# Optimization experiments

Hardware: AMD Instinct MI355X
Metric: run time of the kernel (lower is better)

Reference implementation:

```python
import jax, jax.numpy as jnp
import numpy as np

B, N, D, H = 4, 1024, 1024, 16
DH = D // H
SCALE = jnp.sqrt(jnp.float32(DH))


def setup_inputs() -> dict:
    key = jax.random.key(0)
    ks = jax.random.split(key, 12)
    Q = jax.random.normal(ks[0], (B, N, D), dtype=jnp.float32)
    K = jax.random.normal(ks[1], (B, N, D), dtype=jnp.float32)
    V = jax.random.normal(ks[2], (B, N, D), dtype=jnp.float32)
    mask = jax.random.bernoulli(ks[3], 0.1, (B, H, N, N))
    w_scale = 0.02
    Wq = jax.random.normal(ks[4], (D, D), dtype=jnp.float32) * w_scale
    Wk = jax.random.normal(ks[5], (D, D), dtype=jnp.float32) * w_scale
    Wv = jax.random.normal(ks[6], (D, D), dtype=jnp.float32) * w_scale
    Wo = jax.random.normal(ks[7], (D, D), dtype=jnp.float32) * w_scale
    bq = jax.random.normal(ks[8], (D,), dtype=jnp.float32) * w_scale
    bk = jax.random.normal(ks[9], (D,), dtype=jnp.float32) * w_scale
    bv = jax.random.normal(ks[10], (D,), dtype=jnp.float32) * w_scale
    bo = jax.random.normal(ks[11], (D,), dtype=jnp.float32) * w_scale
    return {"Q": Q, "K": K, "V": V, "mask": mask,
            "Wq": Wq, "bq": bq, "Wk": Wk, "bk": bk,
            "Wv": Wv, "bv": bv, "Wo": Wo, "bo": bo}


def _split_heads(x):
    # [b, n, (h d)] -> [b, h, n, d]
    b, n, _ = x.shape
    return x.reshape(b, n, H, DH).transpose(0, 2, 1, 3)


def reference(Q, K, V, mask, Wq, bq, Wk, bk, Wv, bv, Wo, bo):
    # torch nn.Linear: y = x @ W.T + b
    q = _split_heads(Q @ Wq.T + bq)
    k = _split_heads(K @ Wk.T + bk)
    v = _split_heads(V @ Wv.T + bv)
    # scores: [b, h, n, n]
    scores = jnp.einsum('bhnd,bhmd->bhnm', q, k) / SCALE
    scores = jnp.where(mask, jnp.float32(-1e10), scores)
    weights = jax.nn.softmax(scores, axis=-1)
    attn = jnp.einsum('bhnm,bhmd->bhnd', weights, v)
    x = attn.transpose(0, 2, 1, 3).reshape(Q.shape[0], Q.shape[1], D)
    x = x @ Wo.T + bo
    return (x, weights)
```

## Files before the change

### kernel.cpp

```cpp
#include <hip/hip_runtime.h>


#define SEQ   1024
#define D_DIM 1024
#define HEADS 16
#define DHEAD 64
#define BATCH 4

typedef __attribute__((ext_vector_type(8))) short bhalf8;
typedef __attribute__((ext_vector_type(4))) float floatx4;

static __device__ __forceinline__ unsigned short f2b(float f) {
    unsigned int u = __float_as_uint(f);
    u += 0x7FFFu + ((u >> 16) & 1u);
    return (unsigned short)(u >> 16);
}

__global__ __launch_bounds__(256) void detect_mask_kernel(const uint4* __restrict__ m,
                                                          int* __restrict__ flag) {
    __shared__ int found;
    if (threadIdx.x == 0) found = 0;
    __syncthreads();
    unsigned int bad = 0;
#pragma unroll
    for (int i = 0; i < 16; ++i) {
        uint4 w = m[threadIdx.x + i * 256];
        unsigned int a = w.x, b = w.y, c = w.z, d = w.w;
        bad |= (a != 0u && a != 1u && a != 0x3F800000u);
        bad |= (b != 0u && b != 1u && b != 0x3F800000u);
        bad |= (c != 0u && c != 1u && c != 0x3F800000u);
        bad |= (d != 0u && d != 1u && d != 0x3F800000u);
    }
    if (bad) atomicOr(&found, 1);
    __syncthreads();
    if (threadIdx.x == 0) *flag = found;
}

__global__ __launch_bounds__(256) void mask_pack(const void* __restrict__ mask,
                                                 const int* __restrict__ mflagp,
                                                 unsigned int* __restrict__ bits) {
    const size_t idx = (size_t)blockIdx.x * 256 + threadIdx.x;
    unsigned int w = 0;
    if (*mflagp) {
        const uint4* p = (const uint4*)mask + idx * 2;
        uint4 a = p[0], b = p[1];
        unsigned int d[8] = {a.x, a.y, a.z, a.w, b.x, b.y, b.z, b.w};
#pragma unroll
        for (int i = 0; i < 8; ++i) {
            unsigned int x = d[i];
            w |= (((x & 0x000000FFu) != 0u) ? 1u : 0u) << (i * 4 + 0);
            w |= (((x & 0x0000FF00u) != 0u) ? 1u : 0u) << (i * 4 + 1);
            w |= (((x & 0x00FF0000u) != 0u) ? 1u : 0u) << (i * 4 + 2);
            w |= (((x & 0xFF000000u) != 0u) ? 1u : 0u) << (i * 4 + 3);
        }
    } else {
        const uint4* p = (const uint4*)mask + idx * 8;
#pragma unroll
        for (int i = 0; i < 8; ++i) {
            uint4 a = p[i];
            w |= (a.x ? 1u : 0u) << (i * 4 + 0);
            w |= (a.y ? 1u : 0u) << (i * 4 + 1);
            w |= (a.z ? 1u : 0u) << (i * 4 + 2);
            w |= (a.w ? 1u : 0u) << (i * 4 + 3);
        }
    }
    bits[idx] = w;
}

template <int AMODE, int OMODE>
__global__ __launch_bounds__(256) void gemm_bt(const void* __restrict__ Aptr,
                                               const float* __restrict__ W,
                                               const float* __restrict__ bias,
                                               void* __restrict__ Out) {
    __shared__ unsigned short Al[128 * 72];
    __shared__ unsigned short Bl[128 * 72];

    const int tid = threadIdx.x;
    const int lane = tid & 63, wid = tid >> 6;
    const int lr = lane & 15, lq = lane >> 4;
    const int wm = (wid & 1) * 64, wn = (wid >> 1) * 64;
    const int rowBase = blockIdx.y * 128;
    const int colBase = blockIdx.x * 128;

    floatx4 acc[4][4];
    for (int mi = 0; mi < 4; ++mi)
        for (int ni = 0; ni < 4; ++ni)
            for (int r = 0; r < 4; ++r) acc[mi][ni][r] = 0.f;

    for (int k0 = 0; k0 < D_DIM; k0 += 64) {
        if (AMODE == 0) {
            const float* A = (const float*)Aptr;
            for (int i = 0; i < 8; ++i) {
                int id = tid + i * 256;
                int r = id >> 4, c4 = id & 15;
                float4 f = *(const float4*)&A[(size_t)(rowBase + r) * D_DIM + k0 + c4 * 4];
                ushort4 h;
                h.x = f2b(f.x); h.y = f2b(f.y); h.z = f2b(f.z); h.w = f2b(f.w);
                *(ushort4*)&Al[r * 72 + c4 * 4] = h;
            }
        } else {
            const unsigned short* A = (const unsigned short*)Aptr;
            for (int i = 0; i < 4; ++i) {
                int id = tid + i * 256;
                int r = id >> 3, c8 = id & 7;
                *(uint4*)&Al[r * 72 + c8 * 8] =
                    *(const uint4*)&A[(size_t)(rowBase + r) * D_DIM + k0 + c8 * 8];
            }
        }
        for (int i = 0; i < 8; ++i) {
            int id = tid + i * 256;
            int r = id >> 4, c4 = id & 15;
            float4 f = *(const float4*)&W[(size_t)(colBase + r) * D_DIM + k0 + c4 * 4];
            ushort4 h;
            h.x = f2b(f.x); h.y = f2b(f.y); h.z = f2b(f.z); h.w = f2b(f.w);
            *(ushort4*)&Bl[r * 72 + c4 * 4] = h;
        }
        __syncthreads();
        for (int ks = 0; ks < 2; ++ks) {
            bhalf8 af[4], bfr[4];
            for (int mi = 0; mi < 4; ++mi)
                af[mi] = *(const bhalf8*)&Al[(wm + mi * 16 + lr) * 72 + ks * 32 + lq * 8];
            for (int ni = 0; ni < 4; ++ni)
                bfr[ni] = *(const bhalf8*)&Bl[(wn + ni * 16 + lr) * 72 + ks * 32 + lq * 8];
            for (int mi = 0; mi < 4; ++mi)
                for (int ni = 0; ni < 4; ++ni)
                    acc[mi][ni] = __builtin_amdgcn_mfma_f32_16x16x32_bf16(af[mi], bfr[ni],
                                                                          acc[mi][ni], 0, 0, 0);
        }
        __syncthreads();
    }

    for (int mi = 0; mi < 4; ++mi) {
        for (int ni = 0; ni < 4; ++ni) {
            int col = colBase + wn + ni * 16 + lr;
            float bv = bias[col];
            for (int r = 0; r < 4; ++r) {
                int m = rowBase + wm + mi * 16 + lq * 4 + r;
                float v = acc[mi][ni][r] + bv;
                if (OMODE == 0) {
                    unsigned short* o = (unsigned short*)Out;
                    int b = m >> 10, n = m & 1023, h = col >> 6, dh = col & 63;
                    o[(((size_t)(b * HEADS + h)) << 16) + (n << 6) + dh] = f2b(v);
                } else {
                    float* o = (float*)Out;
                    o[(size_t)m * D_DIM + col] = v;
                }
            }
        }
    }
}

__global__ __launch_bounds__(256, 4) void attn_kernel(const unsigned short* __restrict__ qh,
                                                      const unsigned short* __restrict__ kh,
                                                      const unsigned short* __restrict__ vh,
                                                      const unsigned int* __restrict__ bits,
                                                      float* __restrict__ wout,
                                                      unsigned short* __restrict__ attnb) {
    __shared__ unsigned short ql[64 * 64];
    __shared__ unsigned short kl[64 * 64];
    __shared__ unsigned short vtl[64 * 64];
    __shared__ unsigned short pl[64 * 64];
    __shared__ unsigned int maskw[64 * 32];

    const int tid = threadIdx.x;
    const int lane = tid & 63, wid = tid >> 6;
    const int lr = lane & 15, lq = lane >> 4;

    const int wg = blockIdx.x;
    const int xcd = wg & 7, tt = wg >> 3;
    const int bh = ((tt >> 4) << 3) | xcd;
    const int row0 = (tt & 15) << 6;

    const size_t hoff = (size_t)bh << 16;
    const unsigned short* qp = qh + hoff;
    const unsigned short* kp = kh + hoff;
    const unsigned short* vp = vh + hoff;

#pragma unroll
    for (int i = 0; i < 2; ++i) {
        int id = tid + i * 256;
        int r = id >> 3, c8 = id & 7;
        *(uint4*)&ql[r * 64 + ((c8 ^ (r & 7)) << 3)] =
            *(const uint4*)&qp[((size_t)(row0 + r) << 6) + c8 * 8];
    }
    {
        const unsigned int* src = bits + ((size_t)bh * SEQ + row0) * 32;
#pragma unroll
        for (int i = 0; i < 2; ++i) {
            int id = tid + i * 256;
            *(uint4*)&maskw[id * 4] = *(const uint4*)&src[id * 4];
        }
    }

    uint4 kreg0, kreg1, vreg0, vreg1;
#define LOADK(j)                                                                          \
    {                                                                                     \
        kreg0 = *(const uint4*)&kp[((size_t)(((j) << 6) + (tid >> 3)) << 6) + (tid & 7) * 8];        \
        kreg1 = *(const uint4*)&kp[((size_t)(((j) << 6) + ((tid + 256) >> 3)) << 6) + (tid & 7) * 8]; \
    }
#define STOREK                                                                  \
    {                                                                           \
        int r0 = tid >> 3, c0 = tid & 7, r1 = (tid + 256) >> 3;                 \
        *(uint4*)&kl[r0 * 64 + ((c0 ^ (r0 & 7)) << 3)] = kreg0;                 \
        *(uint4*)&kl[r1 * 64 + ((c0 ^ (r1 & 7)) << 3)] = kreg1;                 \
    }
#define LOADV(j)                                                                          \
    {                                                                                     \
        vreg0 = *(const uint4*)&vp[((size_t)(((j) << 6) + (tid & 63)) << 6) + ((tid >> 6) * 8)];      \
        vreg1 = *(const uint4*)&vp[((size_t)(((j) << 6) + (tid & 63)) << 6) + ((tid >> 6) * 8 + 32)]; \
    }
#define STOREV                                                                  \
    {                                                                           \
        int n0 = tid & 63, d0 = (tid >> 6) * 8, d1 = d0 + 32;                   \
        const unsigned short* e0 = (const unsigned short*)&vreg0;               \
        const unsigned short* e1 = (const unsigned short*)&vreg1;               \
        _Pragma("unroll") for (int t = 0; t < 8; ++t) {                         \
            vtl[(d0 + t) * 64 + (n0 ^ (t << 3))] = e0[t];                       \
            vtl[(d1 + t) * 64 + (n0 ^ (t << 3))] = e1[t];                       \
        }                                                                       \
    }

    float m_l[4], l_l[4];
#pragma unroll
    for (int r = 0; r < 4; ++r) { m_l[r] = -3e38f; l_l[r] = 0.f; }

    LOADK(0);
    for (int j = 0; j < 16; ++j) {
        __syncthreads();
        STOREK;
        if (j < 15) LOADK(j + 1);
        __syncthreads();

        floatx4 sacc[4];
#pragma unroll
        for (int c = 0; c < 4; ++c)
#pragma unroll
            for (int r = 0; r < 4; ++r) sacc[c][r] = 0.f;
#pragma unroll
        for (int ks = 0; ks < 2; ++ks) {
            int arow = wid * 16 + lr;
            bhalf8 a = *(const bhalf8*)&ql[arow * 64 + (((ks * 4 + lq) ^ (lr & 7)) << 3)];
#pragma unroll
            for (int c = 0; c < 4; ++c) {
                int brow = c * 16 + lr;
                bhalf8 bb = *(const bhalf8*)&kl[brow * 64 + (((ks * 4 + lq) ^ (lr & 7)) << 3)];
                sacc[c] = __builtin_amdgcn_mfma_f32_16x16x32_bf16(a, bb, sacc[c], 0, 0, 0);
            }
        }
        unsigned int w0[4], w1[4];
#pragma unroll
        for (int r = 0; r < 4; ++r) {
            int row = wid * 16 + lq * 4 + r;
            w0[r] = maskw[row * 32 + j * 2];
            w1[r] = maskw[row * 32 + j * 2 + 1];
        }
#pragma unroll
        for (int c = 0; c < 4; ++c) {
            int sh = lr + ((c & 1) << 4);
#pragma unroll
            for (int r = 0; r < 4; ++r) {
                unsigned int w = (c >> 1) ? w1[r] : w0[r];
                float s = sacc[c][r] * 0.125f;
                sacc[c][r] = ((w >> sh) & 1u) ? -1e10f : s;
            }
        }
#pragma unroll
        for (int r = 0; r < 4; ++r) {
            float mx = fmaxf(fmaxf(sacc[0][r], sacc[1][r]), fmaxf(sacc[2][r], sacc[3][r]));
            float mn = fmaxf(m_l[r], mx);
            float sv = __expf(sacc[0][r] - mn) + __expf(sacc[1][r] - mn) +
                       __expf(sacc[2][r] - mn) + __expf(sacc[3][r] - mn);
            l_l[r] = l_l[r] * __expf(m_l[r] - mn) + sv;
            m_l[r] = mn;
        }
    }
#pragma unroll
    for (int o = 1; o < 16; o <<= 1) {
#pragma unroll
        for (int r = 0; r < 4; ++r) {
            float mo = __shfl_xor(m_l[r], o);
            float lo = __shfl_xor(l_l[r], o);
            float mn = fmaxf(m_l[r], mo);
            l_l[r] = l_l[r] * __expf(m_l[r] - mn) + lo * __expf(mo - mn);
            m_l[r] = mn;
        }
    }
    float invl[4];
#pragma unroll
    for (int r = 0; r < 4; ++r) invl[r] = 1.f / l_l[r];

    floatx4 oacc[4];
#pragma unroll
    for (int c = 0; c < 4; ++c)
#pragma unroll
        for (int r = 0; r < 4; ++r) oacc[c][r] = 0.f;
    const size_t wrowbase = ((size_t)bh * SEQ + row0) * SEQ;

    LOADK(0);
    LOADV(0);
    for (int j = 0; j < 16; ++j) {
        __syncthreads();
        STOREK;
        STOREV;
        if (j < 15) { LOADK(j + 1); LOADV(j + 1); }
        __syncthreads();

        floatx4 sacc[4];
#pragma unroll
        for (int c = 0; c < 4; ++c)
#pragma unroll
            for (int r = 0; r < 4; ++r) sacc[c][r] = 0.f;
#pragma unroll
        for (int ks = 0; ks < 2; ++ks) {
            int arow = wid * 16 + lr;
            bhalf8 a = *(const bhalf8*)&ql[arow * 64 + (((ks * 4 + lq) ^ (lr & 7)) << 3)];
#pragma unroll
            for (int c = 0; c < 4; ++c) {
                int brow = c * 16 + lr;
                bhalf8 bb = *(const bhalf8*)&kl[brow * 64 + (((ks * 4 + lq) ^ (lr & 7)) << 3)];
                sacc[c] = __builtin_amdgcn_mfma_f32_16x16x32_bf16(a, bb, sacc[c], 0, 0, 0);
            }
        }
        unsigned int w0[4], w1[4];
#pragma unroll
        for (int r = 0; r < 4; ++r) {
            int row = wid * 16 + lq * 4 + r;
            w0[r] = maskw[row * 32 + j * 2];
            w1[r] = maskw[row * 32 + j * 2 + 1];
        }
#pragma unroll
        for (int c = 0; c < 4; ++c) {
            int sh = lr + ((c & 1) << 4);
            int col = (j << 6) + c * 16 + lr;
#pragma unroll
            for (int r = 0; r < 4; ++r) {
                unsigned int w = (c >> 1) ? w1[r] : w0[r];
                int row = wid * 16 + lq * 4 + r;
                float s = sacc[c][r] * 0.125f;
                if ((w >> sh) & 1u) s = -1e10f;
                float p = __expf(s - m_l[r]) * invl[r];
                wout[wrowbase + (size_t)row * SEQ + col] = p;
                pl[row * 64 + ((c * 16 + lr) ^ ((row & 7) << 3))] = f2b(p);
            }
        }
#pragma unroll
        for (int ks = 0; ks < 2; ++ks) {
            int arow = wid * 16 + lr;
            bhalf8 a = *(const bhalf8*)&pl[arow * 64 + (((ks * 4 + lq) ^ (lr & 7)) << 3)];
#pragma unroll
            for (int c = 0; c < 4; ++c) {
                int brow = c * 16 + lr;
                bhalf8 bb = *(const bhalf8*)&vtl[brow * 64 + (((ks * 4 + lq) ^ (lr & 7)) << 3)];
                oacc[c] = __builtin_amdgcn_mfma_f32_16x16x32_bf16(a, bb, oacc[c], 0, 0, 0);
            }
        }
    }

    const int b = bh >> 4, h = bh & 15;
#pragma unroll
    for (int c = 0; c < 4; ++c) {
        int colg = h * 64 + c * 16 + lr;
#pragma unroll
        for (int r = 0; r < 4; ++r) {
            int n = row0 + wid * 16 + lq * 4 + r;
            attnb[(size_t)(b * SEQ + n) * D_DIM + colg] = f2b(oacc[c][r]);
        }
    }
#undef LOADK
#undef STOREK
#undef LOADV
#undef STOREV
}

extern "C" void kernel_launch(void* const* d_in, const int* in_sizes, int n_in,
                              void* d_out, int out_size, void* d_ws, size_t ws_size,
                              hipStream_t stream) {
    const float* Q = (const float*)d_in[0];
    const float* K = (const float*)d_in[1];
    const float* V = (const float*)d_in[2];
    const void* mask = d_in[3];
    const float* Wq = (const float*)d_in[4];
    const float* bq = (const float*)d_in[5];
    const float* Wk = (const float*)d_in[6];
    const float* bk = (const float*)d_in[7];
    const float* Wv = (const float*)d_in[8];
    const float* bv = (const float*)d_in[9];
    const float* Wo = (const float*)d_in[10];
    const float* bo = (const float*)d_in[11];

    char* ws = (char*)d_ws;
    int* mflag = (int*)ws;
    unsigned short* qhb = (unsigned short*)(ws + 256);
    unsigned short* khb = qhb + 4194304;
    unsigned short* vhb = khb + 4194304;
    unsigned short* attnb = vhb + 4194304;
    unsigned int* bitsbuf = (unsigned int*)(attnb + 4194304);

    float* xout = (float*)d_out;
    float* wout = xout + (size_t)BATCH * SEQ * D_DIM;

    dim3 blk(256);
    detect_mask_kernel<<<1, blk, 0, stream>>>((const uint4*)mask, mflag);
    mask_pack<<<dim3(8192), blk, 0, stream>>>(mask, mflag, bitsbuf);

    dim3 g(8, 32);
    gemm_bt<0, 0><<<g, blk, 0, stream>>>(Q, Wq, bq, qhb);
    gemm_bt<0, 0><<<g, blk, 0, stream>>>(K, Wk, bk, khb);
    gemm_bt<0, 0><<<g, blk, 0, stream>>>(V, Wv, bv, vhb);

    attn_kernel<<<dim3(1024), blk, 0, stream>>>(qhb, khb, vhb, bitsbuf, wout, attnb);

    gemm_bt<1, 1><<<g, blk, 0, stream>>>(attnb, Wo, bo, xout);
}
```

Measured before the change: 714.2 us.

## Pre-cast GEMM operands to bf16 and stream tiles with direct global-to-LDS loads

New measurement: 645.8 us. 9.6% less time.

```diff
diff --git a/kernel.cpp b/kernel.cpp
--- a/kernel.cpp
+++ b/kernel.cpp
@@ -10,10 +10,17 @@
 typedef __attribute__((ext_vector_type(8))) short bhalf8;
 typedef __attribute__((ext_vector_type(4))) float floatx4;
 
+typedef __attribute__((address_space(1))) const void GlobCV;
+typedef __attribute__((address_space(3))) void LdsV;
+
 static __device__ __forceinline__ unsigned short f2b(float f) {
     unsigned int u = __float_as_uint(f);
     u += 0x7FFFu + ((u >> 16) & 1u);
     return (unsigned short)(u >> 16);
+}
+
+static __device__ __forceinline__ void gload16(const void* g, void* l) {
+    __builtin_amdgcn_global_load_lds((GlobCV*)g, (LdsV*)l, 16, 0, 0);
 }
 
 __global__ __launch_bounds__(256) void detect_mask_kernel(const uint4* __restrict__ m,
@@ -67,13 +74,48 @@
     bits[idx] = w;
 }
 
-template <int AMODE, int OMODE>
-__global__ __launch_bounds__(256) void gemm_bt(const void* __restrict__ Aptr,
-                                               const float* __restrict__ W,
-                                               const float* __restrict__ bias,
-                                               void* __restrict__ Out) {
-    __shared__ unsigned short Al[128 * 72];
-    __shared__ unsigned short Bl[128 * 72];
+__global__ __launch_bounds__(256) void cast_f2b_all(const float* __restrict__ Q,
+                                                    const float* __restrict__ K,
+                                                    const float* __restrict__ V,
+                                                    const float* __restrict__ Wq,
+                                                    const float* __restrict__ Wk,
+                                                    const float* __restrict__ Wv,
+                                                    const float* __restrict__ Wo,
+                                                    unsigned short* __restrict__ Ab,
+                                                    unsigned short* __restrict__ Wb) {
+    const int y = blockIdx.y;
+    const float* src;
+    unsigned short* dst;
+    int nblocks;
+    if (y < 3) {
+        src = (y == 0) ? Q : (y == 1) ? K : V;
+        dst = Ab + ((size_t)y << 22);
+        nblocks = 2048;
+    } else {
+        src = (y == 3) ? Wq : (y == 4) ? Wk : (y == 5) ? Wv : Wo;
+        dst = Wb + ((size_t)(y - 3) << 20);
+        nblocks = 512;
+    }
+    if (blockIdx.x >= (unsigned)nblocks) return;
+    const size_t i = ((size_t)blockIdx.x * 256 + threadIdx.x) * 8;
+    float4 f0 = *(const float4*)&src[i];
+    float4 f1 = *(const float4*)&src[i + 4];
+    ushort4 h0, h1;
+    h0.x = f2b(f0.x); h0.y = f2b(f0.y); h0.z = f2b(f0.z); h0.w = f2b(f0.w);
+    h1.x = f2b(f1.x); h1.y = f2b(f1.y); h1.z = f2b(f1.z); h1.w = f2b(f1.w);
+    *(ushort4*)&dst[i] = h0;
+    *(ushort4*)&dst[i + 4] = h1;
+}
+
+template <int OMODE>
+__global__ __launch_bounds__(256) void gemm_lds(const unsigned short* __restrict__ Abase,
+                                                const unsigned short* __restrict__ Wbase,
+                                                const float* __restrict__ b0,
+                                                const float* __restrict__ b1,
+                                                const float* __restrict__ b2,
+                                                void* __restrict__ Obase) {
+    __shared__ unsigned short Al[128 * 64];
+    __shared__ unsigned short Bl[128 * 64];
 
     const int tid = threadIdx.x;
     const int lane = tid & 63, wid = tid >> 6;
@@ -81,48 +123,49 @@
     const int wm = (wid & 1) * 64, wn = (wid >> 1) * 64;
     const int rowBase = blockIdx.y * 128;
     const int colBase = blockIdx.x * 128;
+    const int z = blockIdx.z;
+
+    const unsigned short* A = Abase + ((size_t)z << 22);
+    const unsigned short* W = Wbase + ((size_t)z << 20);
+    const float* bias = (z == 0) ? b0 : (z == 1) ? b1 : b2;
+
+    const int srow = lane >> 3;
+    const int scol = (lane & 7) * 8;
 
     floatx4 acc[4][4];
+#pragma unroll
     for (int mi = 0; mi < 4; ++mi)
+#pragma unroll
         for (int ni = 0; ni < 4; ++ni)
+#pragma unroll
             for (int r = 0; r < 4; ++r) acc[mi][ni][r] = 0.f;
 
     for (int k0 = 0; k0 < D_DIM; k0 += 64) {
-        if (AMODE == 0) {
-            const float* A = (const float*)Aptr;
-            for (int i = 0; i < 8; ++i) {
-                int id = tid + i * 256;
-                int r = id >> 4, c4 = id & 15;
-                float4 f = *(const float4*)&A[(size_t)(rowBase + r) * D_DIM + k0 + c4 * 4];
-                ushort4 h;
-                h.x = f2b(f.x); h.y = f2b(f.y); h.z = f2b(f.z); h.w = f2b(f.w);
-                *(ushort4*)&Al[r * 72 + c4 * 4] = h;
-            }
-        } else {
-            const unsigned short* A = (const unsigned short*)Aptr;
-            for (int i = 0; i < 4; ++i) {
-                int id = tid + i * 256;
-                int r = id >> 3, c8 = id & 7;
-                *(uint4*)&Al[r * 72 + c8 * 8] =
-                    *(const uint4*)&A[(size_t)(rowBase + r) * D_DIM + k0 + c8 * 8];
-            }
-        }
-        for (int i = 0; i < 8; ++i) {
-            int id = tid + i * 256;
-            int r = id >> 4, c4 = id & 15;
-            float4 f = *(const float4*)&W[(size_t)(colBase + r) * D_DIM + k0 + c4 * 4];
-            ushort4 h;
-            h.x = f2b(f.x); h.y = f2b(f.y); h.z = f2b(f.z); h.w = f2b(f.w);
-            *(ushort4*)&Bl[r * 72 + c4 * 4] = h;
-        }
-        __syncthreads();
+#pragma unroll
+        for (int i = 0; i < 4; ++i) {
+            int chunk = wid * 4 + i;
+            gload16(&A[(size_t)(rowBase + chunk * 8 + srow) * D_DIM + k0 + scol],
+                    &Al[chunk * 512]);
+        }
+#pragma unroll
+        for (int i = 0; i < 4; ++i) {
+            int chunk = wid * 4 + i;
+            gload16(&W[(size_t)(colBase + chunk * 8 + srow) * D_DIM + k0 + scol],
+                    &Bl[chunk * 512]);
+        }
+        __syncthreads();
+#pragma unroll
         for (int ks = 0; ks < 2; ++ks) {
             bhalf8 af[4], bfr[4];
+#pragma unroll
             for (int mi = 0; mi < 4; ++mi)
-                af[mi] = *(const bhalf8*)&Al[(wm + mi * 16 + lr) * 72 + ks * 32 + lq * 8];
+                af[mi] = *(const bhalf8*)&Al[(wm + mi * 16 + lr) * 64 + ks * 32 + lq * 8];
+#pragma unroll
             for (int ni = 0; ni < 4; ++ni)
-                bfr[ni] = *(const bhalf8*)&Bl[(wn + ni * 16 + lr) * 72 + ks * 32 + lq * 8];
+                bfr[ni] = *(const bhalf8*)&Bl[(wn + ni * 16 + lr) * 64 + ks * 32 + lq * 8];
+#pragma unroll
             for (int mi = 0; mi < 4; ++mi)
+#pragma unroll
                 for (int ni = 0; ni < 4; ++ni)
                     acc[mi][ni] = __builtin_amdgcn_mfma_f32_16x16x32_bf16(af[mi], bfr[ni],
                                                                           acc[mi][ni], 0, 0, 0);
@@ -130,19 +173,22 @@
         __syncthreads();
     }
 
+#pragma unroll
     for (int mi = 0; mi < 4; ++mi) {
+#pragma unroll
         for (int ni = 0; ni < 4; ++ni) {
             int col = colBase + wn + ni * 16 + lr;
             float bv = bias[col];
+#pragma unroll
             for (int r = 0; r < 4; ++r) {
                 int m = rowBase + wm + mi * 16 + lq * 4 + r;
                 float v = acc[mi][ni][r] + bv;
                 if (OMODE == 0) {
-                    unsigned short* o = (unsigned short*)Out;
+                    unsigned short* o = (unsigned short*)Obase + ((size_t)z << 22);
                     int b = m >> 10, n = m & 1023, h = col >> 6, dh = col & 63;
                     o[(((size_t)(b * HEADS + h)) << 16) + (n << 6) + dh] = f2b(v);
                 } else {
-                    float* o = (float*)Out;
+                    float* o = (float*)Obase;
                     o[(size_t)m * D_DIM + col] = v;
                 }
             }
@@ -395,6 +441,10 @@
     unsigned short* vhb = khb + 4194304;
     unsigned short* attnb = vhb + 4194304;
     unsigned int* bitsbuf = (unsigned int*)(attnb + 4194304);
+    unsigned short* Wbf = (unsigned short*)(bitsbuf + 2097152);
+
+    unsigned short* Abf =
+        (unsigned short*)((char*)d_out + (size_t)out_size - (size_t)3 * 4194304 * 2);
 
     float* xout = (float*)d_out;
     float* wout = xout + (size_t)BATCH * SEQ * D_DIM;
@@ -402,13 +452,11 @@
     dim3 blk(256);
     detect_mask_kernel<<<1, blk, 0, stream>>>((const uint4*)mask, mflag);
     mask_pack<<<dim3(8192), blk, 0, stream>>>(mask, mflag, bitsbuf);
-
-    dim3 g(8, 32);
-    gemm_bt<0, 0><<<g, blk, 0, stream>>>(Q, Wq, bq, qhb);
-    gemm_bt<0, 0><<<g, blk, 0, stream>>>(K, Wk, bk, khb);
-    gemm_bt<0, 0><<<g, blk, 0, stream>>>(V, Wv, bv, vhb);
+    cast_f2b_all<<<dim3(2048, 7), blk, 0, stream>>>(Q, K, V, Wq, Wk, Wv, Wo, Abf, Wbf);
+
+    gemm_lds<0><<<dim3(8, 32, 3), blk, 0, stream>>>(Abf, Wbf, bq, bk, bv, qhb);
 
     attn_kernel<<<dim3(1024), blk, 0, stream>>>(qhb, khb, vhb, bitsbuf, wout, attnb);
 
-    gemm_bt<1, 1><<<g, blk, 0, stream>>>(attnb, Wo, bo, xout);
-}
+    gemm_lds<1><<<dim3(8, 32, 1), blk, 0, stream>>>(attnb, Wbf + 3 * 1048576, bo, bo, bo, xout);
+}
```
